# Kernel optimization log

Measured on AMD Instinct MI355X. Metric: run time of the kernel, lower is better.

The kernel has to match this reference:

```python
import jax, jax.numpy as jnp
import numpy as np
from jax import lax

HID = 32  # hardcoded hid_dim in the module

def setup_inputs() -> dict:
    key = jax.random.key(0)
    ks = jax.random.split(key, 12)
    B, HIST, C, F = 512, 24, 184, 17
    PRED = 24
    IN_DIM = HIST + F  # 41
    inp = {
        "pm25_hist": jax.random.normal(ks[0], (B, HIST, C, 1), jnp.float32),
        "feature": jax.random.normal(ks[1], (B, HIST + PRED, C, F), jnp.float32),
        "time_feature": jax.random.normal(ks[2], (B, HIST + PRED, 4), jnp.float32),
        # fc_in: Linear(in_dim, 32)
        "W_in": jax.random.normal(ks[3], (HID, IN_DIM), jnp.float32) / np.sqrt(IN_DIM),
        "b_in": jnp.zeros((HID,), jnp.float32),
        # LSTMCell(32, 32): gate order i, f, g, o
        "W_ih": jax.random.normal(ks[4], (4 * HID, HID), jnp.float32) / np.sqrt(HID),
        "W_hh": jax.random.normal(ks[5], (4 * HID, HID), jnp.float32) / np.sqrt(HID),
        "b_ih": jnp.zeros((4 * HID,), jnp.float32),
        "b_hh": jnp.zeros((4 * HID,), jnp.float32),
        # fc_out: Linear(32, 1)
        "W_out": jax.random.normal(ks[6], (1, HID), jnp.float32) / np.sqrt(HID),
        "b_out": jnp.zeros((1,), jnp.float32),
    }
    return inp

def _forward(pm25_hist, feature, W_in, b_in, W_ih, W_hh, b_ih, b_hh, W_out, b_out):
    B, HIST, C, _ = pm25_hist.shape
    PRED = feature.shape[1] - HIST
    # torch: pm25_hist.reshape(B, C, -1) -- raw row-major reinterpret, same in jnp
    xn0 = pm25_hist.reshape(B, C, HIST)
    h0 = jnp.zeros((B * C, HID), pm25_hist.dtype)
    c0 = jnp.zeros((B * C, HID), pm25_hist.dtype)
    # future features, time-major for scan: [PRED, B, C, F]
    feats = jnp.moveaxis(feature[:, HIST:HIST + PRED], 1, 0)

    def step(carry, feat_t):
        xn, h, c = carry
        x = jnp.concatenate([xn, feat_t], axis=-1)          # [B, C, in_dim]
        x = x @ W_in.T + b_in                               # [B, C, HID]
        xf = x.reshape(B * C, HID)
        gates = xf @ W_ih.T + b_ih + h @ W_hh.T + b_hh      # [B*C, 4*HID]
        i, f, g, o = jnp.split(gates, 4, axis=-1)
        i = jax.nn.sigmoid(i); f = jax.nn.sigmoid(f)
        g = jnp.tanh(g);       o = jax.nn.sigmoid(o)
        c = f * c + i * g
        h = o * jnp.tanh(c)
        pred = h.reshape(B, C, HID) @ W_out.T + b_out       # [B, C, 1]
        xn = jnp.concatenate([xn[:, :, 1:], pred], axis=-1)
        return (xn, h, c), pred

    _, preds = lax.scan(step, (xn0, h0, c0), feats)
    return jnp.moveaxis(preds, 0, 1)  # [B, PRED, C, 1]

def reference(pm25_hist, feature, time_feature, W_in, b_in, W_ih, W_hh, b_ih, b_hh, W_out, b_out):
    # time_feature is accepted but unused, matching the torch module
    return _forward(pm25_hist, feature, W_in, b_in, W_ih, W_hh, b_ih, b_hh, W_out, b_out)
```

## Files before the change

kernel.cpp:

```cpp
#include <hip/hip_runtime.h>
#include <hip/hip_bf16.h>


#define BN     512
#define HISTN  24
#define CNN    184
#define FN     17
#define PREDN  24
#define HIDN   32
#define INN    41
#define CELLS  (BN * CNN)
#define FROW   (CNN * FN)
#define PMROW  (HISTN * CNN)

typedef __attribute__((ext_vector_type(8))) short  short8;
typedef __attribute__((ext_vector_type(4))) float  float4v;

#define MFMA_B16(a, b, c) __builtin_amdgcn_mfma_f32_16x16x32_bf16(a, b, c, 0, 0, 0)

__device__ __forceinline__ short f2bf(float f) {
  union { float f; unsigned u; } v; v.f = f;
  unsigned r = v.u + 0x7fffu + ((v.u >> 16) & 1u);
  return (short)(r >> 16);
}

__device__ __forceinline__ float fast_sigmoid(float x) {
  float e = __expf(-x);
  return __builtin_amdgcn_rcpf(1.0f + e);
}
__device__ __forceinline__ float fast_tanh(float x) {
  float e = __expf(2.0f * x);
  return 1.0f - 2.0f * __builtin_amdgcn_rcpf(1.0f + e);
}

__device__ __forceinline__ int swz(int m, int k) {
  return (((k >> 3) ^ (m & 7)) << 3) | (k & 7);
}
__device__ __forceinline__ short8 rdfrag(const short* rowp, int m, int octl) {
  return *(const short8*)(rowp + ((octl ^ (m & 7)) << 3));
}

__global__ __launch_bounds__(256, 2)
void lstm_fused(const float* __restrict__ pm25,
                const float* __restrict__ feat,
                const float* __restrict__ W_in,  const float* __restrict__ b_in,
                const float* __restrict__ W_ih,  const float* __restrict__ W_hh,
                const float* __restrict__ b_ih,  const float* __restrict__ b_hh,
                const float* __restrict__ W_out, const float* __restrict__ b_out,
                float* __restrict__ out)
{
  __shared__ __align__(16) short Xs[64][64];
  __shared__ __align__(16) short Zs[64][64];
  __shared__ short buf[64][48];

  const int tid   = threadIdx.x;
  const int w     = tid >> 6;
  const int lane  = tid & 63;
  const int q     = lane >> 4;
  const int c0    = lane & 15;
  const int mb    = w << 4;
  const int cell0 = blockIdx.x << 6;

  short8 WzB[2][8];
  #pragma unroll
  for (int ks = 0; ks < 2; ks++) {
    #pragma unroll
    for (int nt = 0; nt < 8; nt++) {
      short8 f;
      const int g = nt * 16 + c0;
      #pragma unroll
      for (int j = 0; j < 8; j++) {
        const int k = ks * 32 + q * 8 + j;
        const float v = (k < 32) ? W_ih[g * 32 + k] : W_hh[g * 32 + (k - 32)];
        f[j] = f2bf(v);
      }
      WzB[ks][nt] = f;
    }
  }
  short8 WxB[2][2];
  #pragma unroll
  for (int ks = 0; ks < 2; ks++) {
    #pragma unroll
    for (int nt = 0; nt < 2; nt++) {
      short8 f;
      const int j2 = nt * 16 + c0;
      #pragma unroll
      for (int j = 0; j < 8; j++) {
        const int k = ks * 32 + q * 8 + j;
        f[j] = (k < INN) ? f2bf(W_in[j2 * INN + k]) : (short)0;
      }
      WxB[ks][nt] = f;
    }
  }
  float bias_i[2], bias_f[2], bias_g[2], bias_o[2], binr[2], woutr[2];
  #pragma unroll
  for (int s = 0; s < 2; s++) {
    const int j = s * 16 + c0;
    bias_i[s] = b_ih[j]      + b_hh[j];
    bias_f[s] = b_ih[32 + j] + b_hh[32 + j];
    bias_g[s] = b_ih[64 + j] + b_hh[64 + j];
    bias_o[s] = b_ih[96 + j] + b_hh[96 + j];
    binr[s]   = b_in[j];
    woutr[s]  = W_out[j];
  }
  const float bo = b_out[0];

  const int cl  = mb + (lane >> 2);
  const int sub = lane & 3;
  const int cg  = cell0 + cl;
  const int bb  = cg / CNN, cc = cg % CNN;
  const float* featBase = feat + ((size_t)(bb * 48 + HISTN)) * FROW + cc * FN;

  {
    const float* src = pm25 + bb * PMROW + cc * HISTN;
    #pragma unroll
    for (int kk = 0; kk < 6; kk++) {
      const int k = sub * 6 + kk;
      buf[cl][k] = f2bf(src[k]);
    }
    for (int k = 41 + sub; k < 64; k += 4) Xs[cl][swz(cl, k)] = 0;
    for (int k = 32 + sub; k < 64; k += 4) Zs[cl][swz(cl, k)] = 0;
  }

  int outB[4], outC[4];
  #pragma unroll
  for (int r = 0; r < 4; r++) {
    const int cgr = cell0 + mb + q * 4 + r;
    outB[r] = cgr / CNN;
    outC[r] = cgr % CNN;
  }

  float cst[2][4];
  #pragma unroll
  for (int s = 0; s < 2; s++)
    #pragma unroll
    for (int r = 0; r < 4; r++) cst[s][r] = 0.f;

  float fv[5];
  #pragma unroll
  for (int i = 0; i < 5; i++) {
    const int f = sub * 5 + i;
    fv[i] = (f < FN) ? featBase[f] : 0.f;
  }

  #pragma unroll 1
  for (int t = 0; t < PREDN; t++) {
    #pragma unroll
    for (int kk = 0; kk < 6; kk++) {
      const int k = sub * 6 + kk;
      Xs[cl][swz(cl, k)] = buf[cl][t + k];
    }
    #pragma unroll
    for (int i = 0; i < 5; i++) {
      const int f = sub * 5 + i;
      if (f < FN) Xs[cl][swz(cl, 24 + f)] = f2bf(fv[i]);
    }
    if (t < PREDN - 1) {
      const float* p = featBase + (size_t)(t + 1) * FROW;
      #pragma unroll
      for (int i = 0; i < 5; i++) {
        const int f = sub * 5 + i;
        fv[i] = (f < FN) ? p[f] : 0.f;
      }
    }

    const short* xrow = &Xs[mb + c0][0];
    const short8 xa = rdfrag(xrow, mb + c0, q);
    const short8 xb = rdfrag(xrow, mb + c0, 4 + q);
    float4v xh[2];
    #pragma unroll
    for (int nt = 0; nt < 2; nt++) {
      float4v a = {0.f, 0.f, 0.f, 0.f};
      a = MFMA_B16(xa, WxB[0][nt], a);
      a = MFMA_B16(xb, WxB[1][nt], a);
      xh[nt] = a;
    }
    #pragma unroll
    for (int s = 0; s < 2; s++) {
      const int j = s * 16 + c0;
      #pragma unroll
      for (int r = 0; r < 4; r++) {
        const int m = mb + q * 4 + r;
        Zs[m][swz(m, j)] = f2bf(xh[s][r] + binr[s]);
      }
    }

    const short* zrow = &Zs[mb + c0][0];
    const short8 za = rdfrag(zrow, mb + c0, q);
    const short8 zb = rdfrag(zrow, mb + c0, 4 + q);
    float4v acc[8];
    #pragma unroll
    for (int nt = 0; nt < 8; nt++) {
      float4v a = {0.f, 0.f, 0.f, 0.f};
      a = MFMA_B16(za, WzB[0][nt], a);
      a = MFMA_B16(zb, WzB[1][nt], a);
      acc[nt] = a;
    }

    float part[4] = {0.f, 0.f, 0.f, 0.f};
    #pragma unroll
    for (int s = 0; s < 2; s++) {
      const int j = s * 16 + c0;
      #pragma unroll
      for (int r = 0; r < 4; r++) {
        const float iv  = fast_sigmoid(acc[0 + s][r] + bias_i[s]);
        const float ff  = fast_sigmoid(acc[2 + s][r] + bias_f[s]);
        const float gv  = fast_tanh   (acc[4 + s][r] + bias_g[s]);
        const float ov  = fast_sigmoid(acc[6 + s][r] + bias_o[s]);
        const float cn  = ff * cst[s][r] + iv * gv;
        cst[s][r] = cn;
        const float hv = ov * fast_tanh(cn);
        const int m = mb + q * 4 + r;
        Zs[m][swz(m, 32 + j)] = f2bf(hv);
        part[r] += woutr[s] * hv;
      }
    }
    #pragma unroll
    for (int r = 0; r < 4; r++) {
      float p = part[r];
      p += __shfl_xor(p, 1);
      p += __shfl_xor(p, 2);
      p += __shfl_xor(p, 4);
      p += __shfl_xor(p, 8);
      part[r] = p;
    }
    if (c0 == 0) {
      #pragma unroll
      for (int r = 0; r < 4; r++) {
        const float pr = part[r] + bo;
        out[(outB[r] * PREDN + t) * CNN + outC[r]] = pr;
        buf[mb + q * 4 + r][24 + t] = f2bf(pr);
      }
    }
  }
}

extern "C" void kernel_launch(void* const* d_in, const int* in_sizes, int n_in,
                              void* d_out, int out_size, void* d_ws, size_t ws_size,
                              hipStream_t stream) {
  (void)in_sizes; (void)n_in; (void)out_size; (void)d_ws; (void)ws_size;
  const float* pm25  = (const float*)d_in[0];
  const float* feat  = (const float*)d_in[1];
  const float* W_in  = (const float*)d_in[3];
  const float* b_in  = (const float*)d_in[4];
  const float* W_ih  = (const float*)d_in[5];
  const float* W_hh  = (const float*)d_in[6];
  const float* b_ih  = (const float*)d_in[7];
  const float* b_hh  = (const float*)d_in[8];
  const float* W_out = (const float*)d_in[9];
  const float* b_out = (const float*)d_in[10];
  float* out = (float*)d_out;

  lstm_fused<<<dim3(CELLS / 64), dim3(256), 0, stream>>>(
      pm25, feat, W_in, b_in, W_ih, W_hh, b_ih, b_hh, W_out, b_out, out);
}
```

Before: 519.5 us.

## Fold input projection into LSTM gate weights and keep history window in registers

A small pre-kernel folds W_in into W_ih, adds the combined bias as an extra input column fed by a constant one, and prescales all weights by log2(e) so the gates can use exp2 directly. The main kernel then runs one K=96 gate GEMM per step instead of the two-stage x projection plus gate GEMM. The sliding pm25 window now lives in packed bf16 registers and is shifted with lane shuffles, so the Xs, Zs and buf staging in shared memory is gone. Launch bounds are raised to 4 blocks per CU. Folding the two matrices in fp32 before rounding to bf16 changes the rounding path slightly, and the extra launch plus workspace dependence add a small fixed cost.

```diff
diff --git a/kernel.cpp b/kernel.cpp
--- a/kernel.cpp
+++ b/kernel.cpp
@@ -12,9 +12,11 @@
 #define CELLS  (BN * CNN)
 #define FROW   (CNN * FN)
 #define PMROW  (HISTN * CNN)
+#define LOG2E  1.4426950408889634f
 
 typedef __attribute__((ext_vector_type(8))) short  short8;
 typedef __attribute__((ext_vector_type(4))) float  float4v;
+typedef __attribute__((ext_vector_type(4))) int    int4v;
 
 #define MFMA_B16(a, b, c) __builtin_amdgcn_mfma_f32_16x16x32_bf16(a, b, c, 0, 0, 0)
 
@@ -23,200 +25,208 @@
   unsigned r = v.u + 0x7fffu + ((v.u >> 16) & 1u);
   return (short)(r >> 16);
 }
-
-__device__ __forceinline__ float fast_sigmoid(float x) {
-  float e = __expf(-x);
-  return __builtin_amdgcn_rcpf(1.0f + e);
-}
-__device__ __forceinline__ float fast_tanh(float x) {
-  float e = __expf(2.0f * x);
+__device__ __forceinline__ int pack2(short lo, short hi) {
+  return (int)(((unsigned)(unsigned short)lo) | (((unsigned)(unsigned short)hi) << 16));
+}
+__device__ __forceinline__ float sig_s(float y) {
+  return __builtin_amdgcn_rcpf(1.0f + exp2f(-y));
+}
+__device__ __forceinline__ float tanh_s(float y) {
+  const float e = exp2f(y + y);
   return 1.0f - 2.0f * __builtin_amdgcn_rcpf(1.0f + e);
 }
-
-__device__ __forceinline__ int swz(int m, int k) {
-  return (((k >> 3) ^ (m & 7)) << 3) | (k & 7);
-}
-__device__ __forceinline__ short8 rdfrag(const short* rowp, int m, int octl) {
-  return *(const short8*)(rowp + ((octl ^ (m & 7)) << 3));
-}
-
-__global__ __launch_bounds__(256, 2)
+__device__ __forceinline__ float tanh_u(float x) {
+  const float e = exp2f(x * (2.0f * LOG2E));
+  return 1.0f - 2.0f * __builtin_amdgcn_rcpf(1.0f + e);
+}
+
+__global__ void build_weights(const float* __restrict__ W_in, const float* __restrict__ b_in,
+                              const float* __restrict__ W_ih, const float* __restrict__ W_hh,
+                              const float* __restrict__ b_ih, const float* __restrict__ b_hh,
+                              short* __restrict__ wfrag)
+{
+  const int tid = blockIdx.x * 256 + threadIdx.x;
+  if (tid >= 128 * 12) return;
+  const int g  = tid / 12;
+  const int kg = tid % 12;
+  const int k0 = kg * 8;
+
+  float v[8];
+  #pragma unroll
+  for (int j = 0; j < 8; ++j) v[j] = 0.f;
+
+  if (k0 < INN) {
+    for (int m = 0; m < HIDN; ++m) {
+      const float wih = W_ih[g * HIDN + m];
+      #pragma unroll
+      for (int j = 0; j < 8; ++j) {
+        const int k = k0 + j;
+        if (k < INN) v[j] += wih * W_in[m * INN + k];
+      }
+    }
+  }
+  if (k0 <= INN && INN < k0 + 8) {
+    float bv = b_ih[g] + b_hh[g];
+    for (int m = 0; m < HIDN; ++m) bv += W_ih[g * HIDN + m] * b_in[m];
+    v[INN - k0] = bv;
+  }
+  if (k0 >= 64) {
+    #pragma unroll
+    for (int j = 0; j < 8; ++j) v[j] = W_hh[g * HIDN + (k0 + j - 64)];
+  }
+
+  const int f = kg >> 2, q = kg & 3, nt = g >> 4, c0 = g & 15;
+  short* dst = wfrag + (((f * 8 + nt) * 64 + q * 16 + c0) * 8);
+  #pragma unroll
+  for (int j = 0; j < 8; ++j) dst[j] = f2bf(v[j] * LOG2E);
+}
+
+__global__ __launch_bounds__(256, 4)
 void lstm_fused(const float* __restrict__ pm25,
                 const float* __restrict__ feat,
-                const float* __restrict__ W_in,  const float* __restrict__ b_in,
-                const float* __restrict__ W_ih,  const float* __restrict__ W_hh,
-                const float* __restrict__ b_ih,  const float* __restrict__ b_hh,
+                const short* __restrict__ wfrag,
                 const float* __restrict__ W_out, const float* __restrict__ b_out,
                 float* __restrict__ out)
 {
-  __shared__ __align__(16) short Xs[64][64];
-  __shared__ __align__(16) short Zs[64][64];
-  __shared__ short buf[64][48];
+  __shared__ __align__(16) short wlds[2 * 8 * 64 * 8];
+  __shared__ __align__(16) short hlds[4][16][40];
 
   const int tid   = threadIdx.x;
   const int w     = tid >> 6;
   const int lane  = tid & 63;
   const int q     = lane >> 4;
   const int c0    = lane & 15;
-  const int mb    = w << 4;
   const int cell0 = blockIdx.x << 6;
-
-  short8 WzB[2][8];
-  #pragma unroll
-  for (int ks = 0; ks < 2; ks++) {
-    #pragma unroll
-    for (int nt = 0; nt < 8; nt++) {
-      short8 f;
-      const int g = nt * 16 + c0;
-      #pragma unroll
-      for (int j = 0; j < 8; j++) {
-        const int k = ks * 32 + q * 8 + j;
-        const float v = (k < 32) ? W_ih[g * 32 + k] : W_hh[g * 32 + (k - 32)];
-        f[j] = f2bf(v);
+  const int mycell = cell0 + (w << 4) + c0;
+
+  {
+    const int4v* src = (const int4v*)(wfrag + 8 * 64 * 8);
+    int4v* dst = (int4v*)wlds;
+    #pragma unroll
+    for (int i = 0; i < 4; ++i) dst[tid + 256 * i] = src[tid + 256 * i];
+  }
+
+  short8 Wka[8];
+  #pragma unroll
+  for (int nt = 0; nt < 8; ++nt)
+    Wka[nt] = *(const short8*)(wfrag + (nt * 64 + lane) * 8);
+
+  float woutr[2];
+  woutr[0] = W_out[c0]; woutr[1] = W_out[16 + c0];
+  const float bo = b_out[0];
+
+  {
+    short* hz = &hlds[w][0][0];
+    for (int i = lane; i < 16 * 40; i += 64) hz[i] = 0;
+  }
+
+  const int bb = mycell / CNN, cc = mycell % CNN;
+
+  int wv[4] = {0, 0, 0, 0};
+  if (q < 3) {
+    const float* src = pm25 + bb * PMROW + cc * HISTN + (q << 3);
+    short tmp[8];
+    #pragma unroll
+    for (int j = 0; j < 8; ++j) tmp[j] = f2bf(src[j]);
+    #pragma unroll
+    for (int i = 0; i < 4; ++i) wv[i] = pack2(tmp[2 * i], tmp[2 * i + 1]);
+  }
+
+  const int pfo = (q == 3) ? 0 : (q == 0) ? 8 : 16;
+  const float* fptr = feat + (size_t)(bb * 48 + HISTN) * FROW + cc * FN + pfo;
+  float pf[8] = {0.f, 0.f, 0.f, 0.f, 0.f, 0.f, 0.f, 0.f};
+  if (q != 2) {
+    if (q == 1) pf[0] = fptr[0];
+    else {
+      #pragma unroll
+      for (int i = 0; i < 8; ++i) pf[i] = fptr[i];
+    }
+  }
+
+  int obase[4];
+  #pragma unroll
+  for (int r = 0; r < 4; ++r) {
+    const int cgr = cell0 + (w << 4) + (q << 2) + r;
+    obase[r] = (cgr / CNN) * (PREDN * CNN) + (cgr % CNN);
+  }
+
+  float cst[2][4] = {{0.f, 0.f, 0.f, 0.f}, {0.f, 0.f, 0.f, 0.f}};
+
+  __syncthreads();
+
+  const char* wl = (const char*)wlds;
+  int wbase = lane * 16;
+  const short* hrd = &hlds[w][c0][q << 3];
+  short* hw = &hlds[w][0][0];
+
+  union WU { int i[4]; short8 v8; };
+
+  #pragma unroll 1
+  for (int t = 0; t < PREDN; ++t) {
+    asm volatile("" : "+v"(wbase));
+
+    WU au;
+    au.i[0] = wv[0]; au.i[1] = wv[1]; au.i[2] = wv[2]; au.i[3] = wv[3];
+    if (q == 3) {
+      #pragma unroll
+      for (int i = 0; i < 4; ++i) au.i[i] = pack2(f2bf(pf[2 * i]), f2bf(pf[2 * i + 1]));
+    }
+    const short8 ka = au.v8;
+
+    WU bu;
+    bu.i[0] = 0; bu.i[1] = 0; bu.i[2] = 0; bu.i[3] = 0;
+    if (q == 0) {
+      #pragma unroll
+      for (int i = 0; i < 4; ++i) bu.i[i] = pack2(f2bf(pf[2 * i]), f2bf(pf[2 * i + 1]));
+    } else if (q == 1) {
+      bu.i[0] = pack2(f2bf(pf[0]), (short)0x3f80);
+    }
+    const short8 kb = bu.v8;
+
+    const short8 kc = *(const short8*)hrd;
+
+    if (t < PREDN - 1 && q != 2) {
+      fptr += FROW;
+      if (q == 1) pf[0] = fptr[0];
+      else {
+        #pragma unroll
+        for (int i = 0; i < 8; ++i) pf[i] = fptr[i];
       }
-      WzB[ks][nt] = f;
-    }
-  }
-  short8 WxB[2][2];
-  #pragma unroll
-  for (int ks = 0; ks < 2; ks++) {
-    #pragma unroll
-    for (int nt = 0; nt < 2; nt++) {
-      short8 f;
-      const int j2 = nt * 16 + c0;
-      #pragma unroll
-      for (int j = 0; j < 8; j++) {
-        const int k = ks * 32 + q * 8 + j;
-        f[j] = (k < INN) ? f2bf(W_in[j2 * INN + k]) : (short)0;
-      }
-      WxB[ks][nt] = f;
-    }
-  }
-  float bias_i[2], bias_f[2], bias_g[2], bias_o[2], binr[2], woutr[2];
-  #pragma unroll
-  for (int s = 0; s < 2; s++) {
-    const int j = s * 16 + c0;
-    bias_i[s] = b_ih[j]      + b_hh[j];
-    bias_f[s] = b_ih[32 + j] + b_hh[32 + j];
-    bias_g[s] = b_ih[64 + j] + b_hh[64 + j];
-    bias_o[s] = b_ih[96 + j] + b_hh[96 + j];
-    binr[s]   = b_in[j];
-    woutr[s]  = W_out[j];
-  }
-  const float bo = b_out[0];
-
-  const int cl  = mb + (lane >> 2);
-  const int sub = lane & 3;
-  const int cg  = cell0 + cl;
-  const int bb  = cg / CNN, cc = cg % CNN;
-  const float* featBase = feat + ((size_t)(bb * 48 + HISTN)) * FROW + cc * FN;
-
-  {
-    const float* src = pm25 + bb * PMROW + cc * HISTN;
-    #pragma unroll
-    for (int kk = 0; kk < 6; kk++) {
-      const int k = sub * 6 + kk;
-      buf[cl][k] = f2bf(src[k]);
-    }
-    for (int k = 41 + sub; k < 64; k += 4) Xs[cl][swz(cl, k)] = 0;
-    for (int k = 32 + sub; k < 64; k += 4) Zs[cl][swz(cl, k)] = 0;
-  }
-
-  int outB[4], outC[4];
-  #pragma unroll
-  for (int r = 0; r < 4; r++) {
-    const int cgr = cell0 + mb + q * 4 + r;
-    outB[r] = cgr / CNN;
-    outC[r] = cgr % CNN;
-  }
-
-  float cst[2][4];
-  #pragma unroll
-  for (int s = 0; s < 2; s++)
-    #pragma unroll
-    for (int r = 0; r < 4; r++) cst[s][r] = 0.f;
-
-  float fv[5];
-  #pragma unroll
-  for (int i = 0; i < 5; i++) {
-    const int f = sub * 5 + i;
-    fv[i] = (f < FN) ? featBase[f] : 0.f;
-  }
-
-  #pragma unroll 1
-  for (int t = 0; t < PREDN; t++) {
-    #pragma unroll
-    for (int kk = 0; kk < 6; kk++) {
-      const int k = sub * 6 + kk;
-      Xs[cl][swz(cl, k)] = buf[cl][t + k];
-    }
-    #pragma unroll
-    for (int i = 0; i < 5; i++) {
-      const int f = sub * 5 + i;
-      if (f < FN) Xs[cl][swz(cl, 24 + f)] = f2bf(fv[i]);
-    }
-    if (t < PREDN - 1) {
-      const float* p = featBase + (size_t)(t + 1) * FROW;
-      #pragma unroll
-      for (int i = 0; i < 5; i++) {
-        const int f = sub * 5 + i;
-        fv[i] = (f < FN) ? p[f] : 0.f;
-      }
-    }
-
-    const short* xrow = &Xs[mb + c0][0];
-    const short8 xa = rdfrag(xrow, mb + c0, q);
-    const short8 xb = rdfrag(xrow, mb + c0, 4 + q);
-    float4v xh[2];
-    #pragma unroll
-    for (int nt = 0; nt < 2; nt++) {
-      float4v a = {0.f, 0.f, 0.f, 0.f};
-      a = MFMA_B16(xa, WxB[0][nt], a);
-      a = MFMA_B16(xb, WxB[1][nt], a);
-      xh[nt] = a;
-    }
-    #pragma unroll
-    for (int s = 0; s < 2; s++) {
-      const int j = s * 16 + c0;
-      #pragma unroll
-      for (int r = 0; r < 4; r++) {
-        const int m = mb + q * 4 + r;
-        Zs[m][swz(m, j)] = f2bf(xh[s][r] + binr[s]);
-      }
-    }
-
-    const short* zrow = &Zs[mb + c0][0];
-    const short8 za = rdfrag(zrow, mb + c0, q);
-    const short8 zb = rdfrag(zrow, mb + c0, 4 + q);
+    }
+
+    __builtin_amdgcn_s_setprio(1);
+    const float4v z4 = {0.f, 0.f, 0.f, 0.f};
     float4v acc[8];
     #pragma unroll
-    for (int nt = 0; nt < 8; nt++) {
-      float4v a = {0.f, 0.f, 0.f, 0.f};
-      a = MFMA_B16(za, WzB[0][nt], a);
-      a = MFMA_B16(zb, WzB[1][nt], a);
+    for (int nt = 0; nt < 8; ++nt) {
+      float4v a = MFMA_B16(ka, Wka[nt], z4);
+      const short8 wkb = *(const short8*)(wl + wbase + nt * 1024);
+      a = MFMA_B16(kb, wkb, a);
+      const short8 wkc = *(const short8*)(wl + wbase + 8192 + nt * 1024);
+      a = MFMA_B16(kc, wkc, a);
       acc[nt] = a;
     }
+    __builtin_amdgcn_s_setprio(0);
 
     float part[4] = {0.f, 0.f, 0.f, 0.f};
     #pragma unroll
-    for (int s = 0; s < 2; s++) {
-      const int j = s * 16 + c0;
-      #pragma unroll
-      for (int r = 0; r < 4; r++) {
-        const float iv  = fast_sigmoid(acc[0 + s][r] + bias_i[s]);
-        const float ff  = fast_sigmoid(acc[2 + s][r] + bias_f[s]);
-        const float gv  = fast_tanh   (acc[4 + s][r] + bias_g[s]);
-        const float ov  = fast_sigmoid(acc[6 + s][r] + bias_o[s]);
-        const float cn  = ff * cst[s][r] + iv * gv;
+    for (int s = 0; s < 2; ++s) {
+      #pragma unroll
+      for (int r = 0; r < 4; ++r) {
+        const float iv = sig_s(acc[0 + s][r]);
+        const float fv = sig_s(acc[2 + s][r]);
+        const float gv = tanh_s(acc[4 + s][r]);
+        const float ov = sig_s(acc[6 + s][r]);
+        const float cn = fv * cst[s][r] + iv * gv;
         cst[s][r] = cn;
-        const float hv = ov * fast_tanh(cn);
-        const int m = mb + q * 4 + r;
-        Zs[m][swz(m, 32 + j)] = f2bf(hv);
+        const float hv = ov * tanh_u(cn);
+        hw[((q << 2) + r) * 40 + (s << 4) + c0] = f2bf(hv);
         part[r] += woutr[s] * hv;
       }
     }
-    #pragma unroll
-    for (int r = 0; r < 4; r++) {
+
+    #pragma unroll
+    for (int r = 0; r < 4; ++r) {
       float p = part[r];
       p += __shfl_xor(p, 1);
       p += __shfl_xor(p, 2);
@@ -226,11 +236,22 @@
     }
     if (c0 == 0) {
       #pragma unroll
-      for (int r = 0; r < 4; r++) {
-        const float pr = part[r] + bo;
-        out[(outB[r] * PREDN + t) * CNN + outC[r]] = pr;
-        buf[mb + q * 4 + r][24 + t] = f2bf(pr);
-      }
+      for (int r = 0; r < 4; ++r)
+        out[obase[r] + t * CNN] = part[r] + bo;
+    }
+
+    if (t < PREDN - 1) {
+      const float v01 = (c0 & 1) ? part[1] : part[0];
+      const float v23 = (c0 & 1) ? part[3] : part[2];
+      const float vs  = (c0 & 2) ? v23 : v01;
+      const float pv = __shfl(vs, ((c0 >> 2) << 4) | c0) + bo;
+      const int pw = (int)(unsigned short)f2bf(pv);
+      const int nb = __shfl(wv[0], (lane + 16) & 63);
+      const int inc = (q == 2) ? pw : nb;
+      wv[0] = (int)(((unsigned)wv[0] >> 16) | ((unsigned)wv[1] << 16));
+      wv[1] = (int)(((unsigned)wv[1] >> 16) | ((unsigned)wv[2] << 16));
+      wv[2] = (int)(((unsigned)wv[2] >> 16) | ((unsigned)wv[3] << 16));
+      wv[3] = (int)(((unsigned)wv[3] >> 16) | ((unsigned)inc   << 16));
     }
   }
 }
@@ -238,7 +259,7 @@
 extern "C" void kernel_launch(void* const* d_in, const int* in_sizes, int n_in,
                               void* d_out, int out_size, void* d_ws, size_t ws_size,
                               hipStream_t stream) {
-  (void)in_sizes; (void)n_in; (void)out_size; (void)d_ws; (void)ws_size;
+  (void)in_sizes; (void)n_in; (void)out_size; (void)ws_size;
   const float* pm25  = (const float*)d_in[0];
   const float* feat  = (const float*)d_in[1];
   const float* W_in  = (const float*)d_in[3];
@@ -251,6 +272,10 @@
   const float* b_out = (const float*)d_in[10];
   float* out = (float*)d_out;
 
+  short* wfrag = (short*)d_ws;
+
+  build_weights<<<dim3(6), dim3(256), 0, stream>>>(
+      W_in, b_in, W_ih, W_hh, b_ih, b_hh, wfrag);
   lstm_fused<<<dim3(CELLS / 64), dim3(256), 0, stream>>>(
-      pm25, feat, W_in, b_in, W_ih, W_hh, b_ih, b_hh, W_out, b_out, out);
-}
+      pm25, feat, wfrag, W_out, b_out, out);
+}
```

Result: slower. 535.5 us (+3.1%).
